# Kernel tuning notes

Hardware: AMD Instinct MI355X
Metric: run time of the kernel (lower is better)

## Reference

```python
import jax, jax.numpy as jnp
import numpy as np

N_NODES = 50000
N_EDGES = 800000
HID = 128
DEPTH = 10
N_GRAPHS = 512
IN_F = 32


def setup_inputs() -> dict:
    key = jax.random.key(0)
    ks = jax.random.split(key, 12)
    x = jax.random.normal(ks[0], (N_NODES, IN_F), jnp.float32)
    edge_index = jax.random.randint(ks[1], (2, N_EDGES), 0, N_NODES, dtype=jnp.int32)
    batch_map = jnp.sort(jax.random.randint(ks[2], (N_NODES,), 0, N_GRAPHS, dtype=jnp.int32))
    # parameters (PyG GraphConv: lin_rel has bias, lin_root has no bias)
    W_embed = jax.random.normal(ks[3], (IN_F, HID), jnp.float32) * 0.1
    W_rel = jax.random.normal(ks[4], (DEPTH, HID, HID), jnp.float32) * 0.05
    b_rel = jax.random.normal(ks[5], (DEPTH, HID), jnp.float32) * 0.01
    W_root = jax.random.normal(ks[6], (DEPTH, HID, HID), jnp.float32) * 0.05
    W_ws = jax.random.normal(ks[7], (DEPTH * HID, 1), jnp.float32) * 0.05
    b_ws = jax.random.normal(ks[8], (1,), jnp.float32) * 0.01
    W_sg = jax.random.normal(ks[9], (DEPTH * HID, IN_F), jnp.float32) * 0.05
    b_sg = jax.random.normal(ks[10], (IN_F,), jnp.float32) * 0.01
    return {
        "x": x, "edge_index": edge_index, "batch_map": batch_map,
        "num_graphs": N_GRAPHS,
        "W_embed": W_embed, "W_rel": W_rel, "b_rel": b_rel, "W_root": W_root,
        "W_ws": W_ws, "b_ws": b_ws, "W_sg": W_sg, "b_sg": b_sg,
    }


def reference(x, edge_index, batch_map, num_graphs,
              W_embed, W_rel, b_rel, W_root, W_ws, b_ws, W_sg, b_sg):
    n = x.shape[0]
    src, dst = edge_index[0], edge_index[1]
    h = x @ W_embed  # [N, 128]
    reps = []
    for i in range(DEPTH):
        # PyG GraphConv (aggr='add'): lin_rel(sum_j h_j) + lin_root(h_i)
        agg = jax.ops.segment_sum(h[src], dst, num_segments=n)  # [N, 128]
        h = agg @ W_rel[i] + b_rel[i] + h @ W_root[i]
        reps.append(h)
    out = jnp.concatenate(reps, axis=1)  # [N, 1280]
    # softmax over last dim of [N,1] logits (faithful: yields ones)
    sum_w = jax.nn.softmax(out @ W_ws + b_ws, axis=-1)  # [N, 1]
    out = sum_w * out
    pooled = jax.ops.segment_sum(out, batch_map, num_segments=num_graphs)  # [G, 1280]
    return pooled @ W_sg + b_sg  # [G, 32]
```

## Files before the change

### kernel.cpp

```cpp
#include <hip/hip_runtime.h>

#define N_NODES 50000
#define N_EDGES 800000
#define HID 128
#define DEPTH 10
#define N_GRAPHS 512
#define IN_F 32

#define BM 128
#define GBLK (50048 / BM)
#define PADN 50048

#define ROWW 256

#define SB 256
#define NSB ((N_NODES + SB - 1) / SB)

#define NBIN 8
#define BINW ((N_NODES + NBIN - 1) / NBIN)
#define NCH 125
#define CHSZ (N_EDGES / NCH)

#define NBT 24
#define NAST 16
#define PACK_CHUNKS (DEPTH * NBT * 512)

typedef __attribute__((ext_vector_type(8))) short short8;
typedef __attribute__((ext_vector_type(4))) float f32x4;
typedef __attribute__((ext_vector_type(4))) unsigned uint4v;

__device__ __forceinline__ float bf2f(short u) {
    union { unsigned i; float f; } v; v.i = ((unsigned)(unsigned short)u) << 16; return v.f;
}
__device__ __forceinline__ short f2bf(float f) {
    union { float f; unsigned i; } v; v.f = f;
    unsigned r = (v.i + 0x7FFFu + ((v.i >> 16) & 1u)) >> 16;
    return (short)r;
}
__device__ __forceinline__ unsigned pack2(short lo, short hi) {
    return ((unsigned)(unsigned short)hi << 16) | (unsigned)(unsigned short)lo;
}

__global__ __launch_bounds__(256) void pack_weights(
    const float* __restrict__ Wrel, const float* __restrict__ Wroot,
    short* __restrict__ Bp) {
    int idx = blockIdx.x * 256 + threadIdx.x;
    if (idx >= PACK_CHUNKS) return;
    int layer = idx / (NBT * 512);
    int rem = idx - layer * NBT * 512;
    int t = rem >> 9;
    int c = rem & 511;
    int kslot = c >> 7, n = c & 127;
    int kc, lo;
    const float* W;
    if (t < 8)       { kc = t >> 1;        W = Wrel;  lo = t & 1; }
    else if (t < 12) { kc = t - 8;         W = Wrel;  lo = 0; }
    else if (t < 20) { kc = (t - 12) >> 1; W = Wroot; lo = t & 1; }
    else             { kc = t - 20;        W = Wroot; lo = 0; }
    W += (size_t)layer * HID * HID;
    short out[8];
#pragma unroll
    for (int j = 0; j < 8; ++j) {
        int k = kc * 32 + kslot * 8 + j;
        float v = W[(size_t)k * HID + n];
        short hi = f2bf(v);
        if (lo) { v = v - bf2f(hi); hi = f2bf(v); }
        out[j] = hi;
    }
    *reinterpret_cast<short8*>(Bp + (size_t)idx * 8) = *reinterpret_cast<short8*>(out);
}

__global__ __launch_bounds__(128) void embed_kernel(
    const float* __restrict__ x, const float* __restrict__ W,
    short* __restrict__ hIL, short* __restrict__ hHr) {
    __shared__ float Ws[IN_F * HID];
    int t = threadIdx.x;
    for (int i = t; i < IN_F * HID; i += 128) Ws[i] = W[i];
    __syncthreads();
    int nbeg = blockIdx.x * 50;
    for (int n = nbeg; n < nbeg + 50; ++n) {
        float acc = 0.f;
#pragma unroll
        for (int k = 0; k < IN_F; ++k)
            acc += x[(size_t)n * IN_F + k] * Ws[k * HID + t];
        short hh = f2bf(acc);
        hIL[(size_t)n * ROWW + t] = hh;
        hIL[(size_t)n * ROWW + HID + t] = f2bf(acc - bf2f(hh));
        hHr[(size_t)n * HID + t] = hh;
    }
}

__global__ __launch_bounds__(256) void hist8_kernel(
    const int* __restrict__ dst, int* __restrict__ counts8) {
    int e = blockIdx.x * 256 + threadIdx.x;
    int plane = blockIdx.x & 7;
    if (e < N_EDGES) atomicAdd(&counts8[(size_t)plane * N_NODES + dst[e]], 1);
}

__global__ __launch_bounds__(SB) void scan_part1(
    const int* __restrict__ counts8, int* __restrict__ counts,
    int* __restrict__ bsum, int n) {
    __shared__ int s[SB];
    int t = threadIdx.x;
    int i = blockIdx.x * SB + t;
    int v = 0;
    if (i < n) {
#pragma unroll
        for (int p = 0; p < 8; ++p) v += counts8[(size_t)p * N_NODES + i];
        counts[i] = v;
    }
    s[t] = v;
    __syncthreads();
    for (int off = SB / 2; off >= 1; off >>= 1) {
        if (t < off) s[t] += s[t + off];
        __syncthreads();
    }
    if (t == 0) bsum[blockIdx.x] = s[0];
}

__global__ __launch_bounds__(256) void scan_part2(
    const int* __restrict__ bsum, int* __restrict__ boff, int nb) {
    __shared__ int s[256];
    int t = threadIdx.x;
    int v0 = (t < nb) ? bsum[t] : 0;
    s[t] = v0;
    __syncthreads();
    for (int off = 1; off < 256; off <<= 1) {
        int v = (t >= off) ? s[t - off] : 0;
        __syncthreads();
        s[t] += v;
        __syncthreads();
    }
    boff[t] = (t == 0) ? 0 : s[t - 1];
}

__global__ __launch_bounds__(SB) void scan_part3(
    const int* __restrict__ count, const int* __restrict__ boff,
    int* __restrict__ ptr, int* __restrict__ cursor, int n) {
    __shared__ int s[SB];
    int b = blockIdx.x, t = threadIdx.x;
    int i = b * SB + t;
    int v = (i < n) ? count[i] : 0;
    s[t] = v;
    __syncthreads();
    for (int off = 1; off < SB; off <<= 1) {
        int u = (t >= off) ? s[t - off] : 0;
        __syncthreads();
        s[t] += u;
        __syncthreads();
    }
    int excl = s[t] - v + boff[b];
    if (i < n) {
        ptr[i] = excl;
        cursor[i] = excl;
        if (i == n - 1) ptr[n] = excl + v;
    }
}

__global__ __launch_bounds__(256) void scatter8_kernel(
    const int* __restrict__ src, const int* __restrict__ dst,
    int* __restrict__ cursor, int* __restrict__ sorted_src) {
    int s = blockIdx.x & 7;
    int c = blockIdx.x >> 3;
    int lo = s * BINW;
    int hi = lo + BINW;
    int base = c * CHSZ;
    for (int e = base + threadIdx.x; e < base + CHSZ; e += 256) {
        int d = dst[e];
        int sv = src[e];
        if (d >= lo && d < hi) {
            int p = atomicAdd(&cursor[d], 1);
            sorted_src[p] = sv;
        }
    }
}

__global__ __launch_bounds__(256) void aggregate_kernel(
    const short* __restrict__ hHr, const int* __restrict__ row_ptr,
    const int* __restrict__ sorted_src, short* __restrict__ agg2) {
    int n = (blockIdx.x * 256 + threadIdx.x) >> 6;
    int lane = threadIdx.x & 63;
    const unsigned* __restrict__ R = (const unsigned*)hHr;
    int beg = row_ptr[n], end = row_ptr[n + 1];
    float a0 = 0.f, a1 = 0.f;
#define ACC(v) do { \
        union { unsigned u; float f; } u0, u1; \
        u0.u = (v) << 16; u1.u = (v) & 0xFFFF0000u; \
        a0 += u0.f; a1 += u1.f; } while (0)
    int j = beg;
    for (; j + 8 <= end; j += 8) {
        unsigned v[8];
#pragma unroll
        for (int u = 0; u < 8; ++u) {
            int s = __builtin_amdgcn_readfirstlane(sorted_src[j + u]);
            v[u] = R[(size_t)s * 64 + lane];
        }
#pragma unroll
        for (int u = 0; u < 8; ++u) ACC(v[u]);
    }
    for (; j + 2 <= end; j += 2) {
        int s0 = __builtin_amdgcn_readfirstlane(sorted_src[j]);
        int s1 = __builtin_amdgcn_readfirstlane(sorted_src[j + 1]);
        unsigned v0 = R[(size_t)s0 * 64 + lane];
        unsigned v1 = R[(size_t)s1 * 64 + lane];
        ACC(v0); ACC(v1);
    }
    if (j < end) {
        int s = __builtin_amdgcn_readfirstlane(sorted_src[j]);
        unsigned v = R[(size_t)s * 64 + lane];
        ACC(v);
    }
#undef ACC
    short h0 = f2bf(a0), h1 = f2bf(a1);
    unsigned hw = pack2(h0, h1);
    unsigned lw = pack2(f2bf(a0 - bf2f(h0)), f2bf(a1 - bf2f(h1)));
    ((unsigned*)agg2)[(size_t)n * 128 + lane] = hw;
    ((unsigned*)agg2)[(size_t)n * 128 + 64 + lane] = lw;
}

__global__ __launch_bounds__(512) void layer_gemm_mfma(
    const short* __restrict__ agg2, const short* __restrict__ hIL,
    const short* __restrict__ Bp, const float* __restrict__ bias,
    short* __restrict__ outIL, short* __restrict__ outH,
    const int* __restrict__ bmap, float* __restrict__ pooled, int layer,
    int write_h) {
    __shared__ __align__(16) char smem[49664];
    short* AbBuf = (short*)smem;
    short* BbBuf = (short*)(smem + 16384);
    float* Cs    = (float*)smem;
    int*   bmapS = (int*)(smem + 49152);

    int tid = threadIdx.x;
    int lane = tid & 63;
    int w = tid >> 6;
    int wr = w >> 2, wc = w & 3;
    int m0 = blockIdx.x * BM;

    int r0 = tid >> 2, q0 = tid & 3;

    f32x4 acc[4][2];
#pragma unroll
    for (int m = 0; m < 4; ++m)
#pragma unroll
        for (int n = 0; n < 2; ++n) acc[m][n] = (f32x4)0.f;

#define NB_OF(a)   ((((a) >> 2) & 1) ? 1 : 2)
#define BOFF_OF(a) (((a) < 4) ? (a) * 2 : ((a) < 8) ? 8 + ((a) - 4) \
                    : ((a) < 12) ? 12 + ((a) - 8) * 2 : 20 + ((a) - 12))
#define A_PTR(a) ((((a) >> 2) <= 1 ? agg2 : hIL) + ((((a) >> 2) & 1) ? HID : 0))

    {
        const short* Ap = A_PTR(0);
        short8 a0 = *reinterpret_cast<const short8*>(Ap + (size_t)(m0 + r0) * ROWW + q0 * 8);
        short8 b0 = *reinterpret_cast<const short8*>(Bp + (size_t)tid * 8);
        short8 b1 = *reinterpret_cast<const short8*>(Bp + 4096 * 8 / 8 * 8 + (size_t)tid * 8 + 4096);
        b1 = *reinterpret_cast<const short8*>(Bp + (size_t)4096 + (size_t)tid * 8);
        *reinterpret_cast<short8*>(&AbBuf[(q0 * 128 + r0) * 8]) = a0;
        *reinterpret_cast<short8*>(&BbBuf[tid * 8]) = b0;
        *reinterpret_cast<short8*>(&BbBuf[4096 + tid * 8]) = b1;
    }
    __syncthreads();

    int kb = lane >> 4;
    int rr = lane & 15;

    for (int a = 0; a < NAST; ++a) {
        int cur = a & 1;
        int nb = NB_OF(a);
        short8 an, bn0, bn1;
        int nbn = 0;
        if (a < NAST - 1) {
            int na = a + 1;
            nbn = NB_OF(na);
            int kc = (na & 3) * 32;
            const short* Ap = A_PTR(na) + kc;
            an = *reinterpret_cast<const short8*>(Ap + (size_t)(m0 + r0) * ROWW + q0 * 8);
            const short* Bsrc = Bp + (size_t)BOFF_OF(na) * 4096;
            bn0 = *reinterpret_cast<const short8*>(Bsrc + (size_t)tid * 8);
            if (nbn == 2)
                bn1 = *reinterpret_cast<const short8*>(Bsrc + (size_t)4096 + (size_t)tid * 8);
        }
        short8 af[4];
#pragma unroll
        for (int m = 0; m < 4; ++m)
            af[m] = *reinterpret_cast<const short8*>(&AbBuf[cur * 4096 + (kb * 128 + wr * 64 + m * 16 + rr) * 8]);
#pragma unroll
        for (int j = 0; j < 2; ++j) {
            if (j < nb) {
                short8 bfr[2];
#pragma unroll
                for (int n = 0; n < 2; ++n)
                    bfr[n] = *reinterpret_cast<const short8*>(
                        &BbBuf[cur * 8192 + j * 4096 + (kb * 128 + wc * 32 + n * 16 + rr) * 8]);
#pragma unroll
                for (int m = 0; m < 4; ++m)
#pragma unroll
                    for (int n = 0; n < 2; ++n)
                        acc[m][n] = __builtin_amdgcn_mfma_f32_16x16x32_bf16(af[m], bfr[n], acc[m][n], 0, 0, 0);
            }
        }
        if (a < NAST - 1) {
            int nxt = cur ^ 1;
            *reinterpret_cast<short8*>(&AbBuf[nxt * 4096 + (q0 * 128 + r0) * 8]) = an;
            *reinterpret_cast<short8*>(&BbBuf[nxt * 8192 + tid * 8]) = bn0;
            if (nbn == 2)
                *reinterpret_cast<short8*>(&BbBuf[nxt * 8192 + 4096 + tid * 8]) = bn1;
        }
        __syncthreads();
    }
#undef NB_OF
#undef BOFF_OF
#undef A_PTR

    if (tid < 128) {
        int gi = m0 + tid;
        bmapS[tid] = bmap[gi < N_NODES ? gi : N_NODES - 1];
    }
    float bs[2];
    {
        int col = wc * 32 + rr;
#pragma unroll
        for (int n = 0; n < 2; ++n) bs[n] = bias[col + n * 16];
    }
    int colP = tid & 127;
    int quarter = tid >> 7;

    for (int c = 0; c < 2; ++c) {
        if (wr == c) {
            int colb = wc * 32 + rr;
#pragma unroll
            for (int m = 0; m < 4; ++m) {
#pragma unroll
                for (int n = 0; n < 2; ++n) {
#pragma unroll
                    for (int i = 0; i < 4; ++i) {
                        int lr = m * 16 + kb * 4 + i;
                        Cs[lr * 132 + colb + n * 16] = acc[m][n][i] + bs[n];
                    }
                }
            }
        }
        __syncthreads();

        if (write_h) {
#pragma unroll
            for (int pq = 0; pq < 2; ++pq) {
                int idx = pq * 512 + tid;
                int lr = idx >> 4;
                int oct = idx & 15;
                const float4* crow = reinterpret_cast<const float4*>(&Cs[lr * 132 + oct * 8]);
                float4 c0 = crow[0], c1 = crow[1];
                float v[8] = {c0.x, c0.y, c0.z, c0.w, c1.x, c1.y, c1.z, c1.w};
                unsigned hw[4], lw[4];
#pragma unroll
                for (int k = 0; k < 4; ++k) {
                    short ha = f2bf(v[2 * k]), hb = f2bf(v[2 * k + 1]);
                    short la = f2bf(v[2 * k] - bf2f(ha)), lb = f2bf(v[2 * k + 1] - bf2f(hb));
                    hw[k] = pack2(ha, hb);
                    lw[k] = pack2(la, lb);
                }
                int row = m0 + c * 64 + lr;
                unsigned* oI = (unsigned*)(outIL + (size_t)row * ROWW);
                unsigned* oH = (unsigned*)(outH + (size_t)row * HID);
                uint4v hv; hv.x = hw[0]; hv.y = hw[1]; hv.z = hw[2]; hv.w = hw[3];
                uint4v lv; lv.x = lw[0]; lv.y = lw[1]; lv.z = lw[2]; lv.w = lw[3];
                *reinterpret_cast<uint4v*>(oI + oct * 4) = hv;
                *reinterpret_cast<uint4v*>(oI + 64 + oct * 4) = lv;
                *reinterpret_cast<uint4v*>(oH + oct * 4) = hv;
            }
        }

        {
            float pacc = 0.f;
            int gprev = -1;
            float* pbase = pooled + (size_t)layer * HID + colP;
            for (int q = 0; q < 16; ++q) {
                int lr = quarter * 16 + q;
                int grow = m0 + c * 64 + lr;
                if (grow >= N_NODES) break;
                int g = bmapS[c * 64 + lr];
                float v = Cs[lr * 132 + colP];
                if (g != gprev) {
                    if (gprev >= 0) atomicAdd(pbase + (size_t)gprev * (DEPTH * HID), pacc);
                    gprev = g; pacc = v;
                } else {
                    pacc += v;
                }
            }
            if (gprev >= 0) atomicAdd(pbase + (size_t)gprev * (DEPTH * HID), pacc);
        }
        __syncthreads();
    }
}

__global__ __launch_bounds__(256) void final_kernel(
    const float* __restrict__ pooled, const float* __restrict__ Wsg,
    const float* __restrict__ bsg, float* __restrict__ out) {
    int t = threadIdx.x & 31;
    int g = blockIdx.x * 8 + (threadIdx.x >> 5);
    float acc = bsg[t];
    const float* prow = pooled + (size_t)g * (DEPTH * HID);
    for (int k = 0; k < DEPTH * HID; ++k)
        acc += prow[k] * Wsg[k * IN_F + t];
    out[g * IN_F + t] = acc;
}

extern "C" void kernel_launch(void* const* d_in, const int* in_sizes, int n_in,
                              void* d_out, int out_size, void* d_ws, size_t ws_size,
                              hipStream_t stream) {
    const float* x       = (const float*)d_in[0];
    const int*   edge    = (const int*)d_in[1];
    const int*   bmap    = (const int*)d_in[2];
    const float* W_embed = (const float*)d_in[4];
    const float* W_rel   = (const float*)d_in[5];
    const float* b_rel   = (const float*)d_in[6];
    const float* W_root  = (const float*)d_in[7];
    const float* W_sg    = (const float*)d_in[10];
    const float* b_sg    = (const float*)d_in[11];
    float* out = (float*)d_out;

    const int* src = edge;
    const int* dst = edge + N_EDGES;

    char* ws = (char*)d_ws;
    auto alloc = [&](size_t bytes) -> char* {
        char* p = ws;
        ws += (bytes + 255) & ~(size_t)255;
        return p;
    };
    const size_t rowB = (size_t)PADN * ROWW * 2;
    const size_t hB   = (size_t)PADN * HID * 2;
    short* h_a   = (short*)alloc(rowB);
    short* h_b   = (short*)alloc(rowB);
    short* hHr   = (short*)alloc(hB);
    short* agg2  = (short*)alloc(rowB);
    float* pooled = (float*)alloc((size_t)N_GRAPHS * DEPTH * HID * 4);
    int* counts8    = (int*)alloc((size_t)8 * N_NODES * 4);
    int* counts     = (int*)alloc((size_t)N_NODES * 4);
    int* row_ptr    = (int*)alloc((size_t)(N_NODES + 1) * 4);
    int* cursor     = (int*)alloc((size_t)N_NODES * 4);
    int* sorted_src = (int*)alloc((size_t)N_EDGES * 4);
    int* bsum       = (int*)alloc((size_t)256 * 4);
    int* boff       = (int*)alloc((size_t)256 * 4);
    short* Bpacked  = (short*)alloc((size_t)PACK_CHUNKS * 8 * 2);

    hipMemsetAsync(counts8, 0, (size_t)8 * N_NODES * 4, stream);
    hipMemsetAsync(pooled, 0, (size_t)N_GRAPHS * DEPTH * HID * 4, stream);

    pack_weights<<<(PACK_CHUNKS + 255) / 256, 256, 0, stream>>>(W_rel, W_root, Bpacked);
    embed_kernel<<<1000, 128, 0, stream>>>(x, W_embed, h_a, hHr);

    hist8_kernel<<<(N_EDGES + 255) / 256, 256, 0, stream>>>(dst, counts8);
    scan_part1<<<NSB, SB, 0, stream>>>(counts8, counts, bsum, N_NODES);
    scan_part2<<<1, 256, 0, stream>>>(bsum, boff, NSB);
    scan_part3<<<NSB, SB, 0, stream>>>(counts, boff, row_ptr, cursor, N_NODES);
    scatter8_kernel<<<NBIN * NCH, 256, 0, stream>>>(src, dst, cursor, sorted_src);

    short *hc = h_a, *hn = h_b;
    for (int i = 0; i < DEPTH; ++i) {
        aggregate_kernel<<<(N_NODES + 3) / 4, 256, 0, stream>>>(hHr, row_ptr, sorted_src, agg2);
        layer_gemm_mfma<<<GBLK, 512, 0, stream>>>(agg2, hc,
                                                  Bpacked + (size_t)i * NBT * 4096,
                                                  b_rel + (size_t)i * HID,
                                                  hn, hHr, bmap, pooled, i,
                                                  (i < DEPTH - 1) ? 1 : 0);
        short* t = hc; hc = hn; hn = t;
    }

    final_kernel<<<N_GRAPHS / 8, 256, 0, stream>>>(pooled, W_sg, b_sg, out);
}
```

Baseline: 716.1 us.

## Fuse neighbor aggregation into layer GEMM via LDS and halve row tile

Neighbor aggregation is moved into the per-layer MFMA GEMM kernel. Each block gathers and sums the neighbor rows for its 64 nodes straight into LDS in MFMA operand layout, so the agg2 global round trip and one launch per layer go away. To make this possible the row tile drops from 128 to 64, LDS grows to about 72KB, and the bf16 hidden buffer is double-buffered because blocks now read the previous layer's h while other blocks write the next. The scatter chunk count also rises to 500. The cost is that only 8 warps per block do the gather, the larger LDS footprint may reduce occupancy, and the B weights are reloaded twice as often per row.

Result: slower. 894.8 us (+25.0%).

```diff
diff --git a/kernel.cpp b/kernel.cpp
--- a/kernel.cpp
+++ b/kernel.cpp
@@ -7,7 +7,7 @@
 #define N_GRAPHS 512
 #define IN_F 32
 
-#define BM 128
+#define BM 64
 #define GBLK (50048 / BM)
 #define PADN 50048
 
@@ -18,12 +18,14 @@
 
 #define NBIN 8
 #define BINW ((N_NODES + NBIN - 1) / NBIN)
-#define NCH 125
+#define NCH 500
 #define CHSZ (N_EDGES / NCH)
 
 #define NBT 24
 #define NAST 16
 #define PACK_CHUNKS (DEPTH * NBT * 512)
+
+#define LDS_BYTES 73984
 
 typedef __attribute__((ext_vector_type(8))) short short8;
 typedef __attribute__((ext_vector_type(4))) float f32x4;
@@ -175,60 +177,19 @@
     }
 }
 
-__global__ __launch_bounds__(256) void aggregate_kernel(
-    const short* __restrict__ hHr, const int* __restrict__ row_ptr,
-    const int* __restrict__ sorted_src, short* __restrict__ agg2) {
-    int n = (blockIdx.x * 256 + threadIdx.x) >> 6;
-    int lane = threadIdx.x & 63;
-    const unsigned* __restrict__ R = (const unsigned*)hHr;
-    int beg = row_ptr[n], end = row_ptr[n + 1];
-    float a0 = 0.f, a1 = 0.f;
-#define ACC(v) do { \
-        union { unsigned u; float f; } u0, u1; \
-        u0.u = (v) << 16; u1.u = (v) & 0xFFFF0000u; \
-        a0 += u0.f; a1 += u1.f; } while (0)
-    int j = beg;
-    for (; j + 8 <= end; j += 8) {
-        unsigned v[8];
-#pragma unroll
-        for (int u = 0; u < 8; ++u) {
-            int s = __builtin_amdgcn_readfirstlane(sorted_src[j + u]);
-            v[u] = R[(size_t)s * 64 + lane];
-        }
-#pragma unroll
-        for (int u = 0; u < 8; ++u) ACC(v[u]);
-    }
-    for (; j + 2 <= end; j += 2) {
-        int s0 = __builtin_amdgcn_readfirstlane(sorted_src[j]);
-        int s1 = __builtin_amdgcn_readfirstlane(sorted_src[j + 1]);
-        unsigned v0 = R[(size_t)s0 * 64 + lane];
-        unsigned v1 = R[(size_t)s1 * 64 + lane];
-        ACC(v0); ACC(v1);
-    }
-    if (j < end) {
-        int s = __builtin_amdgcn_readfirstlane(sorted_src[j]);
-        unsigned v = R[(size_t)s * 64 + lane];
-        ACC(v);
-    }
-#undef ACC
-    short h0 = f2bf(a0), h1 = f2bf(a1);
-    unsigned hw = pack2(h0, h1);
-    unsigned lw = pack2(f2bf(a0 - bf2f(h0)), f2bf(a1 - bf2f(h1)));
-    ((unsigned*)agg2)[(size_t)n * 128 + lane] = hw;
-    ((unsigned*)agg2)[(size_t)n * 128 + 64 + lane] = lw;
-}
-
-__global__ __launch_bounds__(512) void layer_gemm_mfma(
-    const short* __restrict__ agg2, const short* __restrict__ hIL,
+__global__ __launch_bounds__(512) void fused_layer(
+    const short* __restrict__ hHr, const short* __restrict__ hIL,
+    const int* __restrict__ row_ptr, const int* __restrict__ sorted_src,
     const short* __restrict__ Bp, const float* __restrict__ bias,
-    short* __restrict__ outIL, short* __restrict__ outH,
+    short* __restrict__ outIL, short* __restrict__ outHr,
     const int* __restrict__ bmap, float* __restrict__ pooled, int layer,
     int write_h) {
-    __shared__ __align__(16) char smem[49664];
-    short* AbBuf = (short*)smem;
-    short* BbBuf = (short*)(smem + 16384);
-    float* Cs    = (float*)smem;
-    int*   bmapS = (int*)(smem + 49152);
+    __shared__ __align__(16) char smem[LDS_BYTES];
+    short* aggLDS = (short*)smem;
+    short* AbBuf  = (short*)(smem + 32768);
+    short* BbBuf  = (short*)(smem + 40960);
+    float* Cs     = (float*)smem;
+    int*   bmapS  = (int*)(smem + 73728);
 
     int tid = threadIdx.x;
     int lane = tid & 63;
@@ -236,54 +197,112 @@
     int wr = w >> 2, wc = w & 3;
     int m0 = blockIdx.x * BM;
 
+    {
+        const unsigned* __restrict__ R = (const unsigned*)hHr;
+        int d = lane;
+        int kcq = d >> 4;
+        int ksl = (d >> 2) & 3;
+        int sub = d & 3;
+        unsigned* aggD = (unsigned*)aggLDS;
+        for (int i = 0; i < 8; ++i) {
+            int r = w * 8 + i;
+            int n = m0 + r;
+            float a0 = 0.f, a1 = 0.f;
+            if (n < N_NODES) {
+                int beg = row_ptr[n], end = row_ptr[n + 1];
+#define ACC(v) do { \
+        union { unsigned u; float f; } u0, u1; \
+        u0.u = (v) << 16; u1.u = (v) & 0xFFFF0000u; \
+        a0 += u0.f; a1 += u1.f; } while (0)
+                int j = beg;
+                for (; j + 8 <= end; j += 8) {
+                    unsigned vv[8];
+#pragma unroll
+                    for (int u = 0; u < 8; ++u) {
+                        int s = __builtin_amdgcn_readfirstlane(sorted_src[j + u]);
+                        vv[u] = R[(size_t)s * 64 + d];
+                    }
+#pragma unroll
+                    for (int u = 0; u < 8; ++u) ACC(vv[u]);
+                }
+                for (; j + 2 <= end; j += 2) {
+                    int s0 = __builtin_amdgcn_readfirstlane(sorted_src[j]);
+                    int s1 = __builtin_amdgcn_readfirstlane(sorted_src[j + 1]);
+                    unsigned v0 = R[(size_t)s0 * 64 + d];
+                    unsigned v1 = R[(size_t)s1 * 64 + d];
+                    ACC(v0); ACC(v1);
+                }
+                if (j < end) {
+                    int s = __builtin_amdgcn_readfirstlane(sorted_src[j]);
+                    unsigned v = R[(size_t)s * 64 + d];
+                    ACC(v);
+                }
+#undef ACC
+            }
+            short h0 = f2bf(a0), h1 = f2bf(a1);
+            unsigned hw = pack2(h0, h1);
+            unsigned lw = pack2(f2bf(a0 - bf2f(h0)), f2bf(a1 - bf2f(h1)));
+            int base = ((kcq * 4 + ksl) * 64 + r) * 4 + sub;
+            aggD[base] = hw;
+            aggD[4096 + base] = lw;
+        }
+    }
+    __syncthreads();
+
+    {
+        short8 b0 = *reinterpret_cast<const short8*>(Bp + (size_t)tid * 8);
+        short8 b1 = *reinterpret_cast<const short8*>(Bp + (size_t)4096 + (size_t)tid * 8);
+        *reinterpret_cast<short8*>(&BbBuf[tid * 8]) = b0;
+        *reinterpret_cast<short8*>(&BbBuf[4096 + tid * 8]) = b1;
+    }
+    __syncthreads();
+
+    int kb = lane >> 4;
+    int rr = lane & 15;
     int r0 = tid >> 2, q0 = tid & 3;
 
-    f32x4 acc[4][2];
-#pragma unroll
-    for (int m = 0; m < 4; ++m)
+    f32x4 acc[2][2];
+#pragma unroll
+    for (int m = 0; m < 2; ++m)
 #pragma unroll
         for (int n = 0; n < 2; ++n) acc[m][n] = (f32x4)0.f;
 
 #define NB_OF(a)   ((((a) >> 2) & 1) ? 1 : 2)
 #define BOFF_OF(a) (((a) < 4) ? (a) * 2 : ((a) < 8) ? 8 + ((a) - 4) \
                     : ((a) < 12) ? 12 + ((a) - 8) * 2 : 20 + ((a) - 12))
-#define A_PTR(a) ((((a) >> 2) <= 1 ? agg2 : hIL) + ((((a) >> 2) & 1) ? HID : 0))
-
-    {
-        const short* Ap = A_PTR(0);
-        short8 a0 = *reinterpret_cast<const short8*>(Ap + (size_t)(m0 + r0) * ROWW + q0 * 8);
-        short8 b0 = *reinterpret_cast<const short8*>(Bp + (size_t)tid * 8);
-        short8 b1 = *reinterpret_cast<const short8*>(Bp + 4096 * 8 / 8 * 8 + (size_t)tid * 8 + 4096);
-        b1 = *reinterpret_cast<const short8*>(Bp + (size_t)4096 + (size_t)tid * 8);
-        *reinterpret_cast<short8*>(&AbBuf[(q0 * 128 + r0) * 8]) = a0;
-        *reinterpret_cast<short8*>(&BbBuf[tid * 8]) = b0;
-        *reinterpret_cast<short8*>(&BbBuf[4096 + tid * 8]) = b1;
-    }
-    __syncthreads();
-
-    int kb = lane >> 4;
-    int rr = lane & 15;
 
     for (int a = 0; a < NAST; ++a) {
         int cur = a & 1;
         int nb = NB_OF(a);
         short8 an, bn0, bn1;
-        int nbn = 0;
+        int nbn = 0, nIsH = 0;
         if (a < NAST - 1) {
             int na = a + 1;
             nbn = NB_OF(na);
+            nIsH = (na >= 8);
             int kc = (na & 3) * 32;
-            const short* Ap = A_PTR(na) + kc;
-            an = *reinterpret_cast<const short8*>(Ap + (size_t)(m0 + r0) * ROWW + q0 * 8);
+            if (nIsH && tid < 256) {
+                const short* Ap = hIL + (((na >> 2) == 3) ? HID : 0) + kc;
+                an = *reinterpret_cast<const short8*>(Ap + (size_t)(m0 + r0) * ROWW + q0 * 8);
+            }
             const short* Bsrc = Bp + (size_t)BOFF_OF(na) * 4096;
             bn0 = *reinterpret_cast<const short8*>(Bsrc + (size_t)tid * 8);
             if (nbn == 2)
                 bn1 = *reinterpret_cast<const short8*>(Bsrc + (size_t)4096 + (size_t)tid * 8);
         }
-        short8 af[4];
-#pragma unroll
-        for (int m = 0; m < 4; ++m)
-            af[m] = *reinterpret_cast<const short8*>(&AbBuf[cur * 4096 + (kb * 128 + wr * 64 + m * 16 + rr) * 8]);
+        short8 af[2];
+        if (a < 8) {
+            int plane = a >> 2, kc = a & 3;
+#pragma unroll
+            for (int m = 0; m < 2; ++m)
+                af[m] = *reinterpret_cast<const short8*>(
+                    &aggLDS[(((plane * 4 + kc) * 4 + kb) * 64 + (wr * 32 + m * 16 + rr)) * 8]);
+        } else {
+#pragma unroll
+            for (int m = 0; m < 2; ++m)
+                af[m] = *reinterpret_cast<const short8*>(
+                    &AbBuf[cur * 2048 + (kb * 64 + (wr * 32 + m * 16 + rr)) * 8]);
+        }
 #pragma unroll
         for (int j = 0; j < 2; ++j) {
             if (j < nb) {
@@ -293,7 +312,7 @@
                     bfr[n] = *reinterpret_cast<const short8*>(
                         &BbBuf[cur * 8192 + j * 4096 + (kb * 128 + wc * 32 + n * 16 + rr) * 8]);
 #pragma unroll
-                for (int m = 0; m < 4; ++m)
+                for (int m = 0; m < 2; ++m)
 #pragma unroll
                     for (int n = 0; n < 2; ++n)
                         acc[m][n] = __builtin_amdgcn_mfma_f32_16x16x32_bf16(af[m], bfr[n], acc[m][n], 0, 0, 0);
@@ -301,7 +320,8 @@
         }
         if (a < NAST - 1) {
             int nxt = cur ^ 1;
-            *reinterpret_cast<short8*>(&AbBuf[nxt * 4096 + (q0 * 128 + r0) * 8]) = an;
+            if (nIsH && tid < 256)
+                *reinterpret_cast<short8*>(&AbBuf[nxt * 2048 + (q0 * 64 + r0) * 8]) = an;
             *reinterpret_cast<short8*>(&BbBuf[nxt * 8192 + tid * 8]) = bn0;
             if (nbn == 2)
                 *reinterpret_cast<short8*>(&BbBuf[nxt * 8192 + 4096 + tid * 8]) = bn1;
@@ -310,86 +330,78 @@
     }
 #undef NB_OF
 #undef BOFF_OF
-#undef A_PTR
-
-    if (tid < 128) {
+
+    if (tid < BM) {
         int gi = m0 + tid;
         bmapS[tid] = bmap[gi < N_NODES ? gi : N_NODES - 1];
     }
-    float bs[2];
     {
-        int col = wc * 32 + rr;
-#pragma unroll
-        for (int n = 0; n < 2; ++n) bs[n] = bias[col + n * 16];
-    }
-    int colP = tid & 127;
-    int quarter = tid >> 7;
-
-    for (int c = 0; c < 2; ++c) {
-        if (wr == c) {
-            int colb = wc * 32 + rr;
-#pragma unroll
-            for (int m = 0; m < 4; ++m) {
-#pragma unroll
-                for (int n = 0; n < 2; ++n) {
-#pragma unroll
-                    for (int i = 0; i < 4; ++i) {
-                        int lr = m * 16 + kb * 4 + i;
-                        Cs[lr * 132 + colb + n * 16] = acc[m][n][i] + bs[n];
-                    }
+        int colb = wc * 32 + rr;
+        float bs[2];
+#pragma unroll
+        for (int n = 0; n < 2; ++n) bs[n] = bias[colb + n * 16];
+#pragma unroll
+        for (int m = 0; m < 2; ++m) {
+#pragma unroll
+            for (int n = 0; n < 2; ++n) {
+#pragma unroll
+                for (int i = 0; i < 4; ++i) {
+                    int lr = wr * 32 + m * 16 + kb * 4 + i;
+                    Cs[lr * 132 + colb + n * 16] = acc[m][n][i] + bs[n];
                 }
             }
         }
-        __syncthreads();
-
-        if (write_h) {
-#pragma unroll
-            for (int pq = 0; pq < 2; ++pq) {
-                int idx = pq * 512 + tid;
-                int lr = idx >> 4;
-                int oct = idx & 15;
-                const float4* crow = reinterpret_cast<const float4*>(&Cs[lr * 132 + oct * 8]);
-                float4 c0 = crow[0], c1 = crow[1];
-                float v[8] = {c0.x, c0.y, c0.z, c0.w, c1.x, c1.y, c1.z, c1.w};
-                unsigned hw[4], lw[4];
-#pragma unroll
-                for (int k = 0; k < 4; ++k) {
-                    short ha = f2bf(v[2 * k]), hb = f2bf(v[2 * k + 1]);
-                    short la = f2bf(v[2 * k] - bf2f(ha)), lb = f2bf(v[2 * k + 1] - bf2f(hb));
-                    hw[k] = pack2(ha, hb);
-                    lw[k] = pack2(la, lb);
-                }
-                int row = m0 + c * 64 + lr;
-                unsigned* oI = (unsigned*)(outIL + (size_t)row * ROWW);
-                unsigned* oH = (unsigned*)(outH + (size_t)row * HID);
-                uint4v hv; hv.x = hw[0]; hv.y = hw[1]; hv.z = hw[2]; hv.w = hw[3];
-                uint4v lv; lv.x = lw[0]; lv.y = lw[1]; lv.z = lw[2]; lv.w = lw[3];
-                *reinterpret_cast<uint4v*>(oI + oct * 4) = hv;
-                *reinterpret_cast<uint4v*>(oI + 64 + oct * 4) = lv;
-                *reinterpret_cast<uint4v*>(oH + oct * 4) = hv;
-            }
-        }
-
-        {
-            float pacc = 0.f;
-            int gprev = -1;
-            float* pbase = pooled + (size_t)layer * HID + colP;
-            for (int q = 0; q < 16; ++q) {
-                int lr = quarter * 16 + q;
-                int grow = m0 + c * 64 + lr;
-                if (grow >= N_NODES) break;
-                int g = bmapS[c * 64 + lr];
-                float v = Cs[lr * 132 + colP];
-                if (g != gprev) {
-                    if (gprev >= 0) atomicAdd(pbase + (size_t)gprev * (DEPTH * HID), pacc);
-                    gprev = g; pacc = v;
-                } else {
-                    pacc += v;
-                }
-            }
-            if (gprev >= 0) atomicAdd(pbase + (size_t)gprev * (DEPTH * HID), pacc);
-        }
-        __syncthreads();
+    }
+    __syncthreads();
+
+    if (write_h) {
+#pragma unroll
+        for (int pq = 0; pq < 2; ++pq) {
+            int idx = pq * 512 + tid;
+            int lr = idx >> 4;
+            int oct = idx & 15;
+            const float4* crow = reinterpret_cast<const float4*>(&Cs[lr * 132 + oct * 8]);
+            float4 c0 = crow[0], c1 = crow[1];
+            float v[8] = {c0.x, c0.y, c0.z, c0.w, c1.x, c1.y, c1.z, c1.w};
+            unsigned hw[4], lw[4];
+#pragma unroll
+            for (int k = 0; k < 4; ++k) {
+                short ha = f2bf(v[2 * k]), hb = f2bf(v[2 * k + 1]);
+                short la = f2bf(v[2 * k] - bf2f(ha)), lb = f2bf(v[2 * k + 1] - bf2f(hb));
+                hw[k] = pack2(ha, hb);
+                lw[k] = pack2(la, lb);
+            }
+            int row = m0 + lr;
+            unsigned* oI = (unsigned*)(outIL + (size_t)row * ROWW);
+            unsigned* oH = (unsigned*)(outHr + (size_t)row * HID);
+            uint4v hv; hv.x = hw[0]; hv.y = hw[1]; hv.z = hw[2]; hv.w = hw[3];
+            uint4v lv; lv.x = lw[0]; lv.y = lw[1]; lv.z = lw[2]; lv.w = lw[3];
+            *reinterpret_cast<uint4v*>(oI + oct * 4) = hv;
+            *reinterpret_cast<uint4v*>(oI + 64 + oct * 4) = lv;
+            *reinterpret_cast<uint4v*>(oH + oct * 4) = hv;
+        }
+    }
+
+    {
+        int colP = tid & 127;
+        int quarter = tid >> 7;
+        float pacc = 0.f;
+        int gprev = -1;
+        float* pbase = pooled + (size_t)layer * HID + colP;
+        for (int q = 0; q < 16; ++q) {
+            int lr = quarter * 16 + q;
+            int grow = m0 + lr;
+            if (grow >= N_NODES) break;
+            int g = bmapS[lr];
+            float v = Cs[lr * 132 + colP];
+            if (g != gprev) {
+                if (gprev >= 0) atomicAdd(pbase + (size_t)gprev * (DEPTH * HID), pacc);
+                gprev = g; pacc = v;
+            } else {
+                pacc += v;
+            }
+        }
+        if (gprev >= 0) atomicAdd(pbase + (size_t)gprev * (DEPTH * HID), pacc);
     }
 }
 
@@ -430,10 +442,10 @@
     };
     const size_t rowB = (size_t)PADN * ROWW * 2;
     const size_t hB   = (size_t)PADN * HID * 2;
-    short* h_a   = (short*)alloc(rowB);
-    short* h_b   = (short*)alloc(rowB);
-    short* hHr   = (short*)alloc(hB);
-    short* agg2  = (short*)alloc(rowB);
+    short* h_a    = (short*)alloc(rowB);
+    short* h_b    = (short*)alloc(rowB);
+    short* hHr_a  = (short*)alloc(hB);
+    short* hHr_b  = (short*)alloc(hB);
     float* pooled = (float*)alloc((size_t)N_GRAPHS * DEPTH * HID * 4);
     int* counts8    = (int*)alloc((size_t)8 * N_NODES * 4);
     int* counts     = (int*)alloc((size_t)N_NODES * 4);
@@ -448,7 +460,7 @@
     hipMemsetAsync(pooled, 0, (size_t)N_GRAPHS * DEPTH * HID * 4, stream);
 
     pack_weights<<<(PACK_CHUNKS + 255) / 256, 256, 0, stream>>>(W_rel, W_root, Bpacked);
-    embed_kernel<<<1000, 128, 0, stream>>>(x, W_embed, h_a, hHr);
+    embed_kernel<<<1000, 128, 0, stream>>>(x, W_embed, h_a, hHr_a);
 
     hist8_kernel<<<(N_EDGES + 255) / 256, 256, 0, stream>>>(dst, counts8);
     scan_part1<<<NSB, SB, 0, stream>>>(counts8, counts, bsum, N_NODES);
@@ -457,14 +469,16 @@
     scatter8_kernel<<<NBIN * NCH, 256, 0, stream>>>(src, dst, cursor, sorted_src);
 
     short *hc = h_a, *hn = h_b;
+    short *hrC = hHr_a, *hrN = hHr_b;
     for (int i = 0; i < DEPTH; ++i) {
-        aggregate_kernel<<<(N_NODES + 3) / 4, 256, 0, stream>>>(hHr, row_ptr, sorted_src, agg2);
-        layer_gemm_mfma<<<GBLK, 512, 0, stream>>>(agg2, hc,
-                                                  Bpacked + (size_t)i * NBT * 4096,
-                                                  b_rel + (size_t)i * HID,
-                                                  hn, hHr, bmap, pooled, i,
-                                                  (i < DEPTH - 1) ? 1 : 0);
-        short* t = hc; hc = hn; hn = t;
+        fused_layer<<<GBLK, 512, 0, stream>>>(hrC, hc, row_ptr, sorted_src,
+                                              Bpacked + (size_t)i * NBT * 4096,
+                                              b_rel + (size_t)i * HID,
+                                              hn, hrN, bmap, pooled, i,
+                                              (i < DEPTH - 1) ? 1 : 0);
+        short* t;
+        t = hc; hc = hn; hn = t;
+        t = hrC; hrC = hrN; hrN = t;
     }
 
     final_kernel<<<N_GRAPHS / 8, 256, 0, stream>>>(pooled, W_sg, b_sg, out);
```

## Drop low-part root GEMM passes, remove duplicate hi buffer, rechunk edge scatter

Applied to the files above, without the earlier changes.

Removes the bf16 low-residual activation term from the root (h @ W_root) product, cutting the MFMA passes from 16 to 12 and the packed weight tiles from 24 to 20 per layer. It also drops the separate compact hi-only h buffer: aggregation now gathers from the hi half of the interleaved row, which saves one write stream per layer but doubles the row stride of the gather. The scatter chunk count is raised from 125 to 500. Root-path accuracy is reduced because only hi(h) is used there.

After: 681.2 us. 1.05x faster.

```diff
diff --git a/kernel.cpp b/kernel.cpp
--- a/kernel.cpp
+++ b/kernel.cpp
@@ -18,11 +18,11 @@
 
 #define NBIN 8
 #define BINW ((N_NODES + NBIN - 1) / NBIN)
-#define NCH 125
+#define NCH 500
 #define CHSZ (N_EDGES / NCH)
 
-#define NBT 24
-#define NAST 16
+#define NBT 20
+#define NAST 12
 #define PACK_CHUNKS (DEPTH * NBT * 512)
 
 typedef __attribute__((ext_vector_type(8))) short short8;
@@ -55,8 +55,7 @@
     const float* W;
     if (t < 8)       { kc = t >> 1;        W = Wrel;  lo = t & 1; }
     else if (t < 12) { kc = t - 8;         W = Wrel;  lo = 0; }
-    else if (t < 20) { kc = (t - 12) >> 1; W = Wroot; lo = t & 1; }
-    else             { kc = t - 20;        W = Wroot; lo = 0; }
+    else             { kc = (t - 12) >> 1; W = Wroot; lo = t & 1; }
     W += (size_t)layer * HID * HID;
     short out[8];
 #pragma unroll
@@ -72,7 +71,7 @@
 
 __global__ __launch_bounds__(128) void embed_kernel(
     const float* __restrict__ x, const float* __restrict__ W,
-    short* __restrict__ hIL, short* __restrict__ hHr) {
+    short* __restrict__ hIL) {
     __shared__ float Ws[IN_F * HID];
     int t = threadIdx.x;
     for (int i = t; i < IN_F * HID; i += 128) Ws[i] = W[i];
@@ -86,7 +85,6 @@
         short hh = f2bf(acc);
         hIL[(size_t)n * ROWW + t] = hh;
         hIL[(size_t)n * ROWW + HID + t] = f2bf(acc - bf2f(hh));
-        hHr[(size_t)n * HID + t] = hh;
     }
 }
 
@@ -176,11 +174,11 @@
 }
 
 __global__ __launch_bounds__(256) void aggregate_kernel(
-    const short* __restrict__ hHr, const int* __restrict__ row_ptr,
+    const short* __restrict__ hIL, const int* __restrict__ row_ptr,
     const int* __restrict__ sorted_src, short* __restrict__ agg2) {
     int n = (blockIdx.x * 256 + threadIdx.x) >> 6;
     int lane = threadIdx.x & 63;
-    const unsigned* __restrict__ R = (const unsigned*)hHr;
+    const unsigned* __restrict__ R = (const unsigned*)hIL;
     int beg = row_ptr[n], end = row_ptr[n + 1];
     float a0 = 0.f, a1 = 0.f;
 #define ACC(v) do { \
@@ -193,7 +191,7 @@
 #pragma unroll
         for (int u = 0; u < 8; ++u) {
             int s = __builtin_amdgcn_readfirstlane(sorted_src[j + u]);
-            v[u] = R[(size_t)s * 64 + lane];
+            v[u] = R[(size_t)s * 128 + lane];
         }
 #pragma unroll
         for (int u = 0; u < 8; ++u) ACC(v[u]);
@@ -201,13 +199,13 @@
     for (; j + 2 <= end; j += 2) {
         int s0 = __builtin_amdgcn_readfirstlane(sorted_src[j]);
         int s1 = __builtin_amdgcn_readfirstlane(sorted_src[j + 1]);
-        unsigned v0 = R[(size_t)s0 * 64 + lane];
-        unsigned v1 = R[(size_t)s1 * 64 + lane];
+        unsigned v0 = R[(size_t)s0 * 128 + lane];
+        unsigned v1 = R[(size_t)s1 * 128 + lane];
         ACC(v0); ACC(v1);
     }
     if (j < end) {
         int s = __builtin_amdgcn_readfirstlane(sorted_src[j]);
-        unsigned v = R[(size_t)s * 64 + lane];
+        unsigned v = R[(size_t)s * 128 + lane];
         ACC(v);
     }
 #undef ACC
@@ -221,7 +219,7 @@
 __global__ __launch_bounds__(512) void layer_gemm_mfma(
     const short* __restrict__ agg2, const short* __restrict__ hIL,
     const short* __restrict__ Bp, const float* __restrict__ bias,
-    short* __restrict__ outIL, short* __restrict__ outH,
+    short* __restrict__ outIL,
     const int* __restrict__ bmap, float* __restrict__ pooled, int layer,
     int write_h) {
     __shared__ __align__(16) char smem[49664];
@@ -244,17 +242,15 @@
 #pragma unroll
         for (int n = 0; n < 2; ++n) acc[m][n] = (f32x4)0.f;
 
-#define NB_OF(a)   ((((a) >> 2) & 1) ? 1 : 2)
-#define BOFF_OF(a) (((a) < 4) ? (a) * 2 : ((a) < 8) ? 8 + ((a) - 4) \
-                    : ((a) < 12) ? 12 + ((a) - 8) * 2 : 20 + ((a) - 12))
-#define A_PTR(a) ((((a) >> 2) <= 1 ? agg2 : hIL) + ((((a) >> 2) & 1) ? HID : 0))
+#define NB_OF(a)   (((a) >> 2) == 1 ? 1 : 2)
+#define BOFF_OF(a) (((a) < 4) ? (a) * 2 : ((a) < 8) ? 8 + ((a) - 4) : 12 + ((a) - 8) * 2)
+#define A_PTR(a)   ((((a) >> 2) <= 1 ? agg2 : hIL) + ((((a) >> 2) == 1) ? HID : 0))
 
     {
         const short* Ap = A_PTR(0);
         short8 a0 = *reinterpret_cast<const short8*>(Ap + (size_t)(m0 + r0) * ROWW + q0 * 8);
         short8 b0 = *reinterpret_cast<const short8*>(Bp + (size_t)tid * 8);
-        short8 b1 = *reinterpret_cast<const short8*>(Bp + 4096 * 8 / 8 * 8 + (size_t)tid * 8 + 4096);
-        b1 = *reinterpret_cast<const short8*>(Bp + (size_t)4096 + (size_t)tid * 8);
+        short8 b1 = *reinterpret_cast<const short8*>(Bp + (size_t)4096 + (size_t)tid * 8);
         *reinterpret_cast<short8*>(&AbBuf[(q0 * 128 + r0) * 8]) = a0;
         *reinterpret_cast<short8*>(&BbBuf[tid * 8]) = b0;
         *reinterpret_cast<short8*>(&BbBuf[4096 + tid * 8]) = b1;
@@ -361,12 +357,10 @@
                 }
                 int row = m0 + c * 64 + lr;
                 unsigned* oI = (unsigned*)(outIL + (size_t)row * ROWW);
-                unsigned* oH = (unsigned*)(outH + (size_t)row * HID);
                 uint4v hv; hv.x = hw[0]; hv.y = hw[1]; hv.z = hw[2]; hv.w = hw[3];
                 uint4v lv; lv.x = lw[0]; lv.y = lw[1]; lv.z = lw[2]; lv.w = lw[3];
                 *reinterpret_cast<uint4v*>(oI + oct * 4) = hv;
                 *reinterpret_cast<uint4v*>(oI + 64 + oct * 4) = lv;
-                *reinterpret_cast<uint4v*>(oH + oct * 4) = hv;
             }
         }
 
@@ -429,11 +423,9 @@
         return p;
     };
     const size_t rowB = (size_t)PADN * ROWW * 2;
-    const size_t hB   = (size_t)PADN * HID * 2;
-    short* h_a   = (short*)alloc(rowB);
-    short* h_b   = (short*)alloc(rowB);
-    short* hHr   = (short*)alloc(hB);
-    short* agg2  = (short*)alloc(rowB);
+    short* h_a    = (short*)alloc(rowB);
+    short* h_b    = (short*)alloc(rowB);
+    short* agg2   = (short*)alloc(rowB);
     float* pooled = (float*)alloc((size_t)N_GRAPHS * DEPTH * HID * 4);
     int* counts8    = (int*)alloc((size_t)8 * N_NODES * 4);
     int* counts     = (int*)alloc((size_t)N_NODES * 4);
@@ -448,7 +440,7 @@
     hipMemsetAsync(pooled, 0, (size_t)N_GRAPHS * DEPTH * HID * 4, stream);
 
     pack_weights<<<(PACK_CHUNKS + 255) / 256, 256, 0, stream>>>(W_rel, W_root, Bpacked);
-    embed_kernel<<<1000, 128, 0, stream>>>(x, W_embed, h_a, hHr);
+    embed_kernel<<<1000, 128, 0, stream>>>(x, W_embed, h_a);
 
     hist8_kernel<<<(N_EDGES + 255) / 256, 256, 0, stream>>>(dst, counts8);
     scan_part1<<<NSB, SB, 0, stream>>>(counts8, counts, bsum, N_NODES);
@@ -458,11 +450,11 @@
 
     short *hc = h_a, *hn = h_b;
     for (int i = 0; i < DEPTH; ++i) {
-        aggregate_kernel<<<(N_NODES + 3) / 4, 256, 0, stream>>>(hHr, row_ptr, sorted_src, agg2);
+        aggregate_kernel<<<(N_NODES + 3) / 4, 256, 0, stream>>>(hc, row_ptr, sorted_src, agg2);
         layer_gemm_mfma<<<GBLK, 512, 0, stream>>>(agg2, hc,
                                                   Bpacked + (size_t)i * NBT * 4096,
                                                   b_rel + (size_t)i * HID,
-                                                  hn, hHr, bmap, pooled, i,
+                                                  hn, bmap, pooled, i,
                                                   (i < DEPTH - 1) ? 1 : 0);
         short* t = hc; hc = hn; hn = t;
     }
```
